# Kernel optimization log

Hardware: AMD Instinct MI355X
Metric: run time of the kernel (lower is better)

## Reference

```python
import jax, jax.numpy as jnp
import numpy as np

RANK, A1, A2, B1, B2 = 64, 64, 64, 64, 64
N_TOKENS = 8192


def _xavier_uniform(key, shape, fan_in, fan_out, dtype=jnp.float32):
    bound = float(np.sqrt(6.0 / (fan_in + fan_out)))
    return jax.random.uniform(key, shape, dtype, -bound, bound)


def setup_inputs() -> dict:
    key = jax.random.key(0)
    kx, ka, kb, kbias = jax.random.split(key, 4)
    x = jax.random.normal(kx, (N_TOKENS, A1 * B1), dtype=jnp.float32)
    # torch xavier on a 3D tensor (rank, d1, d2): fan_in = d1*d2, fan_out = rank*d2
    a = _xavier_uniform(ka, (RANK, A1, A2), A1 * A2, RANK * A2)
    b = _xavier_uniform(kb, (RANK, B1, B2), B1 * B2, RANK * B2)
    bias = jax.random.normal(kbias, (A2 * B2,), dtype=jnp.float32)
    return {"x": x, "a": a, "b": b, "bias": bias}


def reference(x, a, b, bias):
    r, a1, a2 = a.shape
    _, b1, b2 = b.shape
    # w = sum_r kron(a_r, b_r):  w[i*b1+k, j*b2+l] = sum_r a[r,i,j] * b[r,k,l]
    w = jnp.einsum('rij,rkl->ikjl', a, b).reshape(a1 * b1, a2 * b2)
    out = x @ w  # (N, a2*b2)
    return out + bias[None, :]
```

## Files before the change

kernel.cpp:

```cpp
#include <hip/hip_runtime.h>
#include <hip/hip_bf16.h>


#define M_DIM 8192
#define N_DIM 4096
#define K_DIM 4096
#define KT_COUNT 128

typedef __attribute__((ext_vector_type(8))) short short8;
typedef __attribute__((ext_vector_type(4))) float floatx4;

typedef __attribute__((address_space(1))) void gvoid_t;
typedef __attribute__((address_space(3))) void lvoid_t;

static __device__ __forceinline__ void gl_lds16(const void* g, const void* l) {
  __builtin_amdgcn_global_load_lds((gvoid_t*)(unsigned long long)g,
                                   (lvoid_t*)(unsigned int)(unsigned long long)l,
                                   16, 0, 0);
}

static __device__ __forceinline__ unsigned short f2bf(float f) {
  unsigned int u = __builtin_bit_cast(unsigned int, f);
  u = (u + 0x7fffu + ((u >> 16) & 1u)) >> 16;
  return (unsigned short)u;
}

__global__ __launch_bounds__(256) void prep_kernel(
    const float* __restrict__ x, const float* __restrict__ a,
    const float* __restrict__ b, unsigned short* __restrict__ Xp,
    unsigned short* __restrict__ Wp) {
  __shared__ float lds[128 * 33];
  const int bid = blockIdx.x;
  const int t = threadIdx.x;

  if (bid < 2048) {
    const int rg = bid & 255;
    const int i = rg >> 2;
    const int j0 = (rg & 3) * 16;
    const int k0 = (bid >> 8) * 8;

    {
      const int r = t >> 2, jq = t & 3;
      float4 v = ((const float4*)(a + (size_t)r * 4096 + i * 64 + j0))[jq];
      ((float4*)lds)[r * 4 + jq] = v;
    }
    __syncthreads();

    const int l = t & 63;
    const int jj = t >> 6;
    float acc[4][8];
#pragma unroll
    for (int jp = 0; jp < 4; ++jp)
#pragma unroll
      for (int kb = 0; kb < 8; ++kb) acc[jp][kb] = 0.f;

    const float* bb = b + k0 * 64 + l;
#pragma unroll 4
    for (int r = 0; r < 64; ++r) {
      float4 aj = ((const float4*)lds)[r * 4 + jj];
      float bv[8];
#pragma unroll
      for (int kb = 0; kb < 8; ++kb) bv[kb] = bb[(size_t)r * 4096 + kb * 64];
      const float av[4] = {aj.x, aj.y, aj.z, aj.w};
#pragma unroll
      for (int jp = 0; jp < 4; ++jp)
#pragma unroll
        for (int kb = 0; kb < 8; ++kb)
          acc[jp][kb] = fmaf(av[jp], bv[kb], acc[jp][kb]);
    }

    const int kt = (i * 64 + k0) >> 5;
    const int c = (k0 & 31) >> 3;
#pragma unroll
    for (int jp = 0; jp < 4; ++jp) {
      const int j = j0 + jj * 4 + jp;
      const int n = j * 64 + l;
      const int blob = (n >> 7) * KT_COUNT + kt;
      const int pos = c * 128 + (n & 127);
      short8 o;
#pragma unroll
      for (int kb = 0; kb < 8; ++kb) o[kb] = (short)f2bf(acc[jp][kb]);
      *(short8*)(Wp + (size_t)blob * 4096 + pos * 8) = o;
    }
  } else {
    const int pid = bid - 2048;
    const int kt = pid & 127;
    const int M0 = pid >> 7;

    {
      const int row = t >> 1;
      const int half = t & 1;
      const float* src = x + (size_t)(M0 * 128 + row) * K_DIM + kt * 32 + half * 16;
      float v[16];
#pragma unroll
      for (int w = 0; w < 4; ++w) {
        float4 vv = ((const float4*)src)[w];
        v[w * 4 + 0] = vv.x; v[w * 4 + 1] = vv.y;
        v[w * 4 + 2] = vv.z; v[w * 4 + 3] = vv.w;
      }
#pragma unroll
      for (int e = 0; e < 16; ++e) lds[row * 33 + half * 16 + e] = v[e];
    }
    __syncthreads();

    unsigned short* dst = Xp + (size_t)(M0 * KT_COUNT + kt) * 4096;
#pragma unroll
    for (int q = 0; q < 2; ++q) {
      const int p = q * 256 + t;
      const int c = p >> 7, mm = p & 127;
      short8 o;
#pragma unroll
      for (int j = 0; j < 8; ++j) o[j] = (short)f2bf(lds[mm * 33 + c * 8 + j]);
      *(short8*)(dst + p * 8) = o;
    }
  }
}

__global__ __launch_bounds__(256) void gemm_kernel(
    const unsigned short* __restrict__ Xp, const unsigned short* __restrict__ Wp,
    const float* __restrict__ bias, float* __restrict__ out) {
  __shared__ short8 As[512];
  __shared__ short8 Bs[512];

  const int bid = blockIdx.x;
  const int xcd = bid & 7;
  const int pos = bid >> 3;
  const int N0 = xcd * 4 + (pos & 3);
  const int M0 = pos >> 2;

  const int t = threadIdx.x;
  const int wave = t >> 6, lane = t & 63;
  const int l16 = lane & 15, quad = lane >> 4;
  const int wm = wave & 1, wn = wave >> 1;

  floatx4 acc[4][4];
#pragma unroll
  for (int mt = 0; mt < 4; ++mt)
#pragma unroll
    for (int nt = 0; nt < 4; ++nt) acc[mt][nt] = (floatx4){0.f, 0.f, 0.f, 0.f};

  const unsigned short* pa = Xp + (size_t)M0 * KT_COUNT * 4096 + (size_t)t * 8;
  const unsigned short* pb = Wp + (size_t)N0 * KT_COUNT * 4096 + (size_t)t * 8;
  const short8* lA0 = As + wave * 64;
  const short8* lA1 = As + 256 + wave * 64;
  const short8* lB0 = Bs + wave * 64;
  const short8* lB1 = Bs + 256 + wave * 64;

  for (int kt = 0; kt < KT_COUNT; ++kt) {
    __syncthreads();
    gl_lds16(pa, lA0);
    gl_lds16(pa + 2048, lA1);
    gl_lds16(pb, lB0);
    gl_lds16(pb + 2048, lB1);
    pa += 4096;
    pb += 4096;
    __syncthreads();

    short8 af[4], bf[4];
#pragma unroll
    for (int mt = 0; mt < 4; ++mt)
      af[mt] = As[quad * 128 + wm * 64 + mt * 16 + l16];
#pragma unroll
    for (int nt = 0; nt < 4; ++nt)
      bf[nt] = Bs[quad * 128 + wn * 64 + nt * 16 + l16];
#pragma unroll
    for (int mt = 0; mt < 4; ++mt)
#pragma unroll
      for (int nt = 0; nt < 4; ++nt)
        acc[mt][nt] = __builtin_amdgcn_mfma_f32_16x16x32_bf16(
            af[mt], bf[nt], acc[mt][nt], 0, 0, 0);
  }

  const int col_base = N0 * 128 + wn * 64;
  const int row_base = M0 * 128 + wm * 64;
#pragma unroll
  for (int nt = 0; nt < 4; ++nt) {
    const int col = col_base + nt * 16 + l16;
    const float bv = bias[col];
#pragma unroll
    for (int mt = 0; mt < 4; ++mt) {
      floatx4 v = acc[mt][nt];
#pragma unroll
      for (int r4 = 0; r4 < 4; ++r4) {
        const int row = row_base + mt * 16 + quad * 4 + r4;
        out[(size_t)row * N_DIM + col] = v[r4] + bv;
      }
    }
  }
}

extern "C" void kernel_launch(void* const* d_in, const int* in_sizes, int n_in,
                              void* d_out, int out_size, void* d_ws, size_t ws_size,
                              hipStream_t stream) {
  const float* x = (const float*)d_in[0];
  const float* a = (const float*)d_in[1];
  const float* b = (const float*)d_in[2];
  const float* bias = (const float*)d_in[3];
  float* out = (float*)d_out;

  unsigned short* Xp = (unsigned short*)d_ws;
  unsigned short* Wp = Xp + (size_t)M_DIM * K_DIM;

  prep_kernel<<<2048 + 8192, 256, 0, stream>>>(x, a, b, Xp, Wp);
  gemm_kernel<<<2048, 256, 0, stream>>>(Xp, Wp, bias, out);
}
```

Before: 505.9 us.

## Switch GEMM to 32x32x16 MFMA tiles and retile weight-build blocks

The GEMM inner loop moves from 16x16x32 bf16 MFMAs (4x4 tiles per wave) to 32x32x16 MFMAs (2x2 tiles per wave, two k-substeps). This cuts the number of MFMA issues and the LDS fragment reads per k-tile. The epilogue is rewritten for the 32x32 accumulator layout. Separately, the weight-construction part of the prep kernel now has each block handle a full row of j (16 j per thread, 4 k) instead of 4x8, halving its block count. In exchange it writes 8-byte short4 stores instead of 16-byte stores and needs more accumulator registers.

```diff
diff --git a/kernel.cpp b/kernel.cpp
--- a/kernel.cpp
+++ b/kernel.cpp
@@ -8,7 +8,9 @@
 #define KT_COUNT 128
 
 typedef __attribute__((ext_vector_type(8))) short short8;
+typedef __attribute__((ext_vector_type(4))) short short4v;
 typedef __attribute__((ext_vector_type(4))) float floatx4;
+typedef __attribute__((ext_vector_type(16))) float floatx16;
 
 typedef __attribute__((address_space(1))) void gvoid_t;
 typedef __attribute__((address_space(3))) void lvoid_t;
@@ -33,57 +35,65 @@
   const int bid = blockIdx.x;
   const int t = threadIdx.x;
 
-  if (bid < 2048) {
-    const int rg = bid & 255;
-    const int i = rg >> 2;
-    const int j0 = (rg & 3) * 16;
-    const int k0 = (bid >> 8) * 8;
+  if (bid < 1024) {
+    const int i = bid >> 4;
+    const int k0 = (bid & 15) * 4;
 
     {
-      const int r = t >> 2, jq = t & 3;
-      float4 v = ((const float4*)(a + (size_t)r * 4096 + i * 64 + j0))[jq];
-      ((float4*)lds)[r * 4 + jq] = v;
+#pragma unroll
+      for (int q = 0; q < 4; ++q) {
+        const int idx = q * 256 + t;
+        const int r = idx >> 4, jq = idx & 15;
+        float4 v = ((const float4*)(a + (size_t)r * 4096 + i * 64))[jq];
+        ((float4*)lds)[r * 16 + jq] = v;
+      }
     }
     __syncthreads();
 
     const int l = t & 63;
-    const int jj = t >> 6;
-    float acc[4][8];
-#pragma unroll
-    for (int jp = 0; jp < 4; ++jp)
-#pragma unroll
-      for (int kb = 0; kb < 8; ++kb) acc[jp][kb] = 0.f;
+    const int jset = t >> 6;
+    float acc[16][4];
+#pragma unroll
+    for (int jj = 0; jj < 16; ++jj)
+#pragma unroll
+      for (int kb = 0; kb < 4; ++kb) acc[jj][kb] = 0.f;
 
     const float* bb = b + k0 * 64 + l;
-#pragma unroll 4
+#pragma unroll 2
     for (int r = 0; r < 64; ++r) {
-      float4 aj = ((const float4*)lds)[r * 4 + jj];
-      float bv[8];
-#pragma unroll
-      for (int kb = 0; kb < 8; ++kb) bv[kb] = bb[(size_t)r * 4096 + kb * 64];
-      const float av[4] = {aj.x, aj.y, aj.z, aj.w};
-#pragma unroll
-      for (int jp = 0; jp < 4; ++jp)
-#pragma unroll
-        for (int kb = 0; kb < 8; ++kb)
-          acc[jp][kb] = fmaf(av[jp], bv[kb], acc[jp][kb]);
+      float bv[4];
+#pragma unroll
+      for (int kb = 0; kb < 4; ++kb) bv[kb] = bb[(size_t)r * 4096 + kb * 64];
+      float av[16];
+#pragma unroll
+      for (int jq = 0; jq < 4; ++jq) {
+        float4 aj = ((const float4*)lds)[r * 16 + jset * 4 + jq];
+        av[jq * 4 + 0] = aj.x; av[jq * 4 + 1] = aj.y;
+        av[jq * 4 + 2] = aj.z; av[jq * 4 + 3] = aj.w;
+      }
+#pragma unroll
+      for (int jj = 0; jj < 16; ++jj)
+#pragma unroll
+        for (int kb = 0; kb < 4; ++kb)
+          acc[jj][kb] = fmaf(av[jj], bv[kb], acc[jj][kb]);
     }
 
     const int kt = (i * 64 + k0) >> 5;
     const int c = (k0 & 31) >> 3;
-#pragma unroll
-    for (int jp = 0; jp < 4; ++jp) {
-      const int j = j0 + jj * 4 + jp;
+    const int half = (k0 >> 2) & 1;
+#pragma unroll
+    for (int jj = 0; jj < 16; ++jj) {
+      const int j = jset * 16 + jj;
       const int n = j * 64 + l;
       const int blob = (n >> 7) * KT_COUNT + kt;
       const int pos = c * 128 + (n & 127);
-      short8 o;
-#pragma unroll
-      for (int kb = 0; kb < 8; ++kb) o[kb] = (short)f2bf(acc[jp][kb]);
-      *(short8*)(Wp + (size_t)blob * 4096 + pos * 8) = o;
+      short4v o;
+#pragma unroll
+      for (int kb = 0; kb < 4; ++kb) o[kb] = (short)f2bf(acc[jj][kb]);
+      *(short4v*)(Wp + (size_t)blob * 4096 + pos * 8 + half * 4) = o;
     }
   } else {
-    const int pid = bid - 2048;
+    const int pid = bid - 1024;
     const int kt = pid & 127;
     const int M0 = pid >> 7;
 
@@ -130,14 +140,16 @@
 
   const int t = threadIdx.x;
   const int wave = t >> 6, lane = t & 63;
-  const int l16 = lane & 15, quad = lane >> 4;
+  const int l32 = lane & 31, hl = lane >> 5;
   const int wm = wave & 1, wn = wave >> 1;
 
-  floatx4 acc[4][4];
-#pragma unroll
-  for (int mt = 0; mt < 4; ++mt)
-#pragma unroll
-    for (int nt = 0; nt < 4; ++nt) acc[mt][nt] = (floatx4){0.f, 0.f, 0.f, 0.f};
+  floatx16 acc[2][2];
+#pragma unroll
+  for (int mt = 0; mt < 2; ++mt)
+#pragma unroll
+    for (int nt = 0; nt < 2; ++nt)
+#pragma unroll
+      for (int r = 0; r < 16; ++r) acc[mt][nt][r] = 0.f;
 
   const unsigned short* pa = Xp + (size_t)M0 * KT_COUNT * 4096 + (size_t)t * 8;
   const unsigned short* pb = Wp + (size_t)N0 * KT_COUNT * 4096 + (size_t)t * 8;
@@ -156,34 +168,38 @@
     pb += 4096;
     __syncthreads();
 
-    short8 af[4], bf[4];
-#pragma unroll
-    for (int mt = 0; mt < 4; ++mt)
-      af[mt] = As[quad * 128 + wm * 64 + mt * 16 + l16];
-#pragma unroll
-    for (int nt = 0; nt < 4; ++nt)
-      bf[nt] = Bs[quad * 128 + wn * 64 + nt * 16 + l16];
-#pragma unroll
-    for (int mt = 0; mt < 4; ++mt)
-#pragma unroll
-      for (int nt = 0; nt < 4; ++nt)
-        acc[mt][nt] = __builtin_amdgcn_mfma_f32_16x16x32_bf16(
-            af[mt], bf[nt], acc[mt][nt], 0, 0, 0);
+#pragma unroll
+    for (int ks = 0; ks < 2; ++ks) {
+      const int c = ks * 2 + hl;
+      short8 af[2], bf[2];
+#pragma unroll
+      for (int mt = 0; mt < 2; ++mt)
+        af[mt] = As[c * 128 + wm * 64 + mt * 32 + l32];
+#pragma unroll
+      for (int nt = 0; nt < 2; ++nt)
+        bf[nt] = Bs[c * 128 + wn * 64 + nt * 32 + l32];
+#pragma unroll
+      for (int mt = 0; mt < 2; ++mt)
+#pragma unroll
+        for (int nt = 0; nt < 2; ++nt)
+          acc[mt][nt] = __builtin_amdgcn_mfma_f32_32x32x16_bf16(
+              af[mt], bf[nt], acc[mt][nt], 0, 0, 0);
+    }
   }
 
   const int col_base = N0 * 128 + wn * 64;
-  const int row_base = M0 * 128 + wm * 64;
-#pragma unroll
-  for (int nt = 0; nt < 4; ++nt) {
-    const int col = col_base + nt * 16 + l16;
+  const int row_base = M0 * 128 + wm * 64 + 4 * hl;
+#pragma unroll
+  for (int nt = 0; nt < 2; ++nt) {
+    const int col = col_base + nt * 32 + l32;
     const float bv = bias[col];
 #pragma unroll
-    for (int mt = 0; mt < 4; ++mt) {
-      floatx4 v = acc[mt][nt];
-#pragma unroll
-      for (int r4 = 0; r4 < 4; ++r4) {
-        const int row = row_base + mt * 16 + quad * 4 + r4;
-        out[(size_t)row * N_DIM + col] = v[r4] + bv;
+    for (int mt = 0; mt < 2; ++mt) {
+      floatx16 v = acc[mt][nt];
+#pragma unroll
+      for (int r = 0; r < 16; ++r) {
+        const int row = row_base + mt * 32 + (r & 3) + 8 * (r >> 2);
+        out[(size_t)row * N_DIM + col] = v[r] + bv;
       }
     }
   }
@@ -201,6 +217,6 @@
   unsigned short* Xp = (unsigned short*)d_ws;
   unsigned short* Wp = Xp + (size_t)M_DIM * K_DIM;
 
-  prep_kernel<<<2048 + 8192, 256, 0, stream>>>(x, a, b, Xp, Wp);
+  prep_kernel<<<1024 + 8192, 256, 0, stream>>>(x, a, b, Xp, Wp);
   gemm_kernel<<<2048, 256, 0, stream>>>(Xp, Wp, bias, out);
 }
```

Result: slower. 576.5 us (+13.9%).
